# Kernel optimization log

Hardware: AMD Instinct MI355X
Metric: run time of the kernel (lower is better)

The kernel has to match this reference:

```python
import jax, jax.numpy as jnp
import numpy as np

N = 50000      # nodes
E = 1600000    # edges (avg degree 32)
F_IN = 128
HID = 256
C = 40


def setup_inputs() -> dict:
    key = jax.random.key(0)
    ks = jax.random.split(key, 12)
    x = jax.random.normal(ks[0], (N, F_IN), jnp.float32)
    edge_index = jax.random.randint(ks[1], (2, E), 0, N, dtype=jnp.int32)

    def glorot(k, fan_in, fan_out):
        s = jnp.sqrt(2.0 / (fan_in + fan_out)).astype(jnp.float32)
        return jax.random.normal(k, (fan_in, fan_out), jnp.float32) * s

    return {
        "x": x,
        "edge_index": edge_index,
        "W1": glorot(ks[2], F_IN, HID), "b1": jnp.zeros((HID,), jnp.float32),
        "W2": glorot(ks[3], HID, HID),  "b2": jnp.zeros((HID,), jnp.float32),
        "W3": glorot(ks[4], HID, HID),  "b3": jnp.zeros((HID,), jnp.float32),
        "W4": glorot(ks[5], HID, C),    "b4": jnp.zeros((C,), jnp.float32),
    }


def _gcn_conv(x, W, b, src, dst, norm_e, self_norm):
    # PyG GCNConv: h = X W; out_j = sum_i norm_ij * h_i  (+ self-loop term) + b
    h = x @ W                                   # [N, F_out]
    msg = h[src] * norm_e[:, None]              # [E, F_out] gather + scale
    agg = jax.ops.segment_sum(msg, dst, num_segments=N)
    agg = agg + h * self_norm[:, None]          # self-loop contribution
    return agg + b


def reference(x, edge_index, W1, b1, W2, b2, W3, b3, W4, b4):
    src, dst = edge_index[0], edge_index[1]
    # degree on A + I (self-loops added), computed over destination nodes
    deg = jax.ops.segment_sum(jnp.ones((E,), x.dtype), dst, num_segments=N) + 1.0
    inv_sqrt = jax.lax.rsqrt(deg)               # [N]
    norm_e = inv_sqrt[src] * inv_sqrt[dst]      # [E] symmetric norm per edge
    self_norm = inv_sqrt * inv_sqrt             # [N] self-loop norm = 1/deg

    h = jax.nn.relu(_gcn_conv(x, W1, b1, src, dst, norm_e, self_norm))
    h = jax.nn.relu(_gcn_conv(h, W2, b2, src, dst, norm_e, self_norm))
    h = jax.nn.relu(_gcn_conv(h, W3, b3, src, dst, norm_e, self_norm))
    h = _gcn_conv(h, W4, b4, src, dst, norm_e, self_norm)
    return jax.nn.log_softmax(h, axis=1)
```

## Files before the change

kernel.cpp:

```cpp
#include <hip/hip_runtime.h>
#include <hip/hip_fp16.h>
#include <math.h>


typedef _Float16 f16x8 __attribute__((ext_vector_type(8)));
typedef float f32x4 __attribute__((ext_vector_type(4)));

__device__ __forceinline__ __half2 u2h2(unsigned u) {
    union { unsigned u; __half2 h; } v; v.u = u; return v.h;
}
__device__ __forceinline__ unsigned h22u(__half2 h) {
    union { unsigned u; __half2 h; } v; v.h = h; return v.u;
}
__device__ __forceinline__ float hlo(unsigned u) {
    return __half2float(__ushort_as_half((unsigned short)(u & 0xFFFFu)));
}
__device__ __forceinline__ float hhi(unsigned u) {
    return __half2float(__ushort_as_half((unsigned short)(u >> 16)));
}


__global__ __launch_bounds__(256) void count_kernel(const int* __restrict__ dst,
                                                    int* __restrict__ counts,
                                                    int* __restrict__ rank, int E) {
    int e = blockIdx.x * 256 + threadIdx.x;
    if (e < E) rank[e] = atomicAdd(&counts[dst[e]], 1);
}

__global__ __launch_bounds__(256) void scan_phase1(const int* __restrict__ counts,
                                                   int* __restrict__ blockSums, int N) {
    int i = blockIdx.x * 256 + threadIdx.x;
    int v = (i < N) ? counts[i] : 0;
    #pragma unroll
    for (int o = 32; o >= 1; o >>= 1) v += __shfl_xor(v, o, 64);
    __shared__ int ws[4];
    int lane = threadIdx.x & 63, w = threadIdx.x >> 6;
    if (lane == 0) ws[w] = v;
    __syncthreads();
    if (threadIdx.x == 0) blockSums[blockIdx.x] = ws[0] + ws[1] + ws[2] + ws[3];
}

__global__ __launch_bounds__(256) void scan_phase2(int* __restrict__ blockSums, int nb) {
    __shared__ int s[256];
    int tid = threadIdx.x;
    int v = (tid < nb) ? blockSums[tid] : 0;
    s[tid] = v;
    __syncthreads();
    for (int off = 1; off < 256; off <<= 1) {
        int t = (tid >= off) ? s[tid - off] : 0;
        __syncthreads();
        s[tid] += t;
        __syncthreads();
    }
    if (tid < nb) blockSums[tid] = s[tid] - v;
}

__global__ __launch_bounds__(256) void scan_phase3(const int* __restrict__ counts,
                                                   const int* __restrict__ blockSums,
                                                   int* __restrict__ offs,
                                                   float* __restrict__ rsq, int N) {
    __shared__ int s[256];
    int tid = threadIdx.x;
    int i = blockIdx.x * 256 + tid;
    int c = (i < N) ? counts[i] : 0;
    s[tid] = c;
    __syncthreads();
    for (int off = 1; off < 256; off <<= 1) {
        int t = (tid >= off) ? s[tid - off] : 0;
        __syncthreads();
        s[tid] += t;
        __syncthreads();
    }
    if (i < N) {
        int excl = s[tid] - c + blockSums[blockIdx.x];
        offs[i] = excl;
        rsq[i] = rsqrtf((float)c + 1.0f);
        if (i == N - 1) offs[N] = excl + c;
    }
}

__global__ __launch_bounds__(256) void scatter_kernel(const int* __restrict__ src,
                                                      const int* __restrict__ dst,
                                                      const int* __restrict__ rank,
                                                      const int* __restrict__ offs,
                                                      const float* __restrict__ rsq,
                                                      unsigned* __restrict__ epk, int E) {
    int e = blockIdx.x * 256 + threadIdx.x;
    if (e < E) {
        int d = dst[e];
        int s = src[e];
        int pos = offs[d] + rank[e];
        float w = rsq[s] * rsq[d];
        epk[pos] = (unsigned)s |
                   ((unsigned)__half_as_ushort(__float2half_rn(w)) << 16);
    }
}

__global__ __launch_bounds__(256) void prep_kernel(
        const float* __restrict__ x, unsigned short* __restrict__ xb, int nx4,
        const float* __restrict__ W1, const float* __restrict__ W2,
        const float* __restrict__ W3, const float* __restrict__ W4,
        unsigned short* __restrict__ Wt1, unsigned short* __restrict__ Wt2,
        unsigned short* __restrict__ Wt3, unsigned short* __restrict__ Wt4) {
    int i = blockIdx.x * 256 + threadIdx.x;
    if (i < nx4) {
        float4 v = reinterpret_cast<const float4*>(x)[i];
        ushort4 o;
        o.x = __half_as_ushort(__float2half_rn(v.x));
        o.y = __half_as_ushort(__float2half_rn(v.y));
        o.z = __half_as_ushort(__float2half_rn(v.z));
        o.w = __half_as_ushort(__float2half_rn(v.w));
        reinterpret_cast<ushort4*>(xb)[i] = o;
        return;
    }
    int j = i - nx4;
    if (j < 32768) {
        int k = j >> 8, n = j & 255;
        Wt1[n * 128 + k] = __half_as_ushort(__float2half_rn(W1[j]));
    } else if (j < 98304) {
        int t = j - 32768; int k = t >> 8, n = t & 255;
        Wt2[n * 256 + k] = __half_as_ushort(__float2half_rn(W2[t]));
    } else if (j < 163840) {
        int t = j - 98304; int k = t >> 8, n = t & 255;
        Wt3[n * 256 + k] = __half_as_ushort(__float2half_rn(W3[t]));
    } else if (j < 174080) {
        int t = j - 163840; int k = t / 40, n = t - k * 40;
        Wt4[n * 256 + k] = __half_as_ushort(__float2half_rn(W4[t]));
    }
}

template <int H2, bool BIAS, bool RELU>
__global__ __launch_bounds__(256) void agg_f16_kernel(
        const unsigned* __restrict__ G,
        const int* __restrict__ offs,
        const unsigned* __restrict__ epk,
        const float* __restrict__ rsq,
        const float* __restrict__ bias,
        unsigned* __restrict__ out, int N) {
    constexpr int ROWU = 64 * H2;
    constexpr int UNR = 8;
    int lane = threadIdx.x & 63;
    int node = blockIdx.x * 4 + (threadIdx.x >> 6);
    if (node >= N) return;
    const unsigned* base = G + lane * H2;

    __half2 acc[H2];
    #pragma unroll
    for (int i = 0; i < H2; i++) acc[i] = u2h2(0u);

    int e = offs[node], e1 = offs[node + 1];
    for (; e + UNR - 1 < e1; e += UNR) {
        unsigned p[UNR];
        int s[UNR];
        #pragma unroll
        for (int j = 0; j < UNR; j++) { p[j] = epk[e + j]; s[j] = p[j] & 0xFFFFu; }
        unsigned g[UNR][H2];
        #pragma unroll
        for (int j = 0; j < UNR; j++)
            #pragma unroll
            for (int i = 0; i < H2; i++)
                g[j][i] = base[(size_t)s[j] * ROWU + i];
        #pragma unroll
        for (int j = 0; j < UNR; j++) {
            __half2 w2 = __half2half2(__ushort_as_half((unsigned short)(p[j] >> 16)));
            #pragma unroll
            for (int i = 0; i < H2; i++)
                acc[i] = __hfma2(w2, u2h2(g[j][i]), acc[i]);
        }
    }
    for (; e < e1; e++) {
        unsigned p0 = epk[e];
        int s0 = p0 & 0xFFFFu;
        __half2 w2 = __half2half2(__ushort_as_half((unsigned short)(p0 >> 16)));
        #pragma unroll
        for (int i = 0; i < H2; i++)
            acc[i] = __hfma2(w2, u2h2(base[(size_t)s0 * ROWU + i]), acc[i]);
    }

    float sn = rsq[node];
    sn *= sn;
    #pragma unroll
    for (int i = 0; i < H2; i++) {
        unsigned sv = base[(size_t)node * ROWU + i];
        float2 f = __half22float2(acc[i]);
        f.x = fmaf(sn, hlo(sv), f.x);
        f.y = fmaf(sn, hhi(sv), f.y);
        if (BIAS) {
            float2 b = reinterpret_cast<const float2*>(bias)[lane * H2 + i];
            f.x += b.x; f.y += b.y;
        }
        if (RELU) { f.x = fmaxf(f.x, 0.f); f.y = fmaxf(f.y, 0.f); }
        out[(size_t)node * ROWU + lane * H2 + i] = h22u(__floats2half2_rn(f.x, f.y));
    }
}

__global__ __launch_bounds__(256) void agg40_softmax_kernel(
        const unsigned* __restrict__ G,
        const int* __restrict__ offs,
        const unsigned* __restrict__ epk,
        const float* __restrict__ rsq,
        const float* __restrict__ bias,
        float* __restrict__ out, int N) {
    int lane = threadIdx.x & 63;
    int node = blockIdx.x * 4 + (threadIdx.x >> 6);
    if (node >= N) return;
    bool act = lane < 20;
    int cl = act ? lane : 0;
    __half2 acch = u2h2(0u);
    int e = offs[node], e1 = offs[node + 1];
    for (; e + 3 < e1; e += 4) {
        unsigned p[4];
        int s[4];
        #pragma unroll
        for (int j = 0; j < 4; j++) { p[j] = epk[e + j]; s[j] = p[j] & 0xFFFFu; }
        unsigned g[4];
        #pragma unroll
        for (int j = 0; j < 4; j++) g[j] = G[(size_t)s[j] * 20 + cl];
        #pragma unroll
        for (int j = 0; j < 4; j++) {
            __half2 w = __half2half2(__ushort_as_half((unsigned short)(p[j] >> 16)));
            acch = __hfma2(w, u2h2(g[j]), acch);
        }
    }
    for (; e < e1; e++) {
        unsigned p0 = epk[e];
        int s0 = p0 & 0xFFFFu;
        __half2 w0 = __half2half2(__ushort_as_half((unsigned short)(p0 >> 16)));
        acch = __hfma2(w0, u2h2(G[(size_t)s0 * 20 + cl]), acch);
    }
    float lo = 0.f, hi = 0.f;
    if (act) {
        float sn = rsq[node];
        sn *= sn;
        unsigned sv = G[(size_t)node * 20 + lane];
        float2 f = __half22float2(acch);
        lo = fmaf(sn, hlo(sv), f.x) + bias[2 * lane];
        hi = fmaf(sn, hhi(sv), f.y) + bias[2 * lane + 1];
    }
    float m = act ? fmaxf(lo, hi) : -INFINITY;
    #pragma unroll
    for (int o = 32; o >= 1; o >>= 1) m = fmaxf(m, __shfl_xor(m, o, 64));
    float s = act ? (expf(lo - m) + expf(hi - m)) : 0.f;
    #pragma unroll
    for (int o = 32; o >= 1; o >>= 1) s += __shfl_xor(s, o, 64);
    float ls = logf(s);
    if (act) {
        float2 o2;
        o2.x = lo - m - ls;
        o2.y = hi - m - ls;
        *reinterpret_cast<float2*>(out + (size_t)node * 40 + 2 * lane) = o2;
    }
}

template <bool BIAS, bool RELU>
__global__ __launch_bounds__(256) void gemm_f16(
        const unsigned short* __restrict__ A,
        const unsigned short* __restrict__ Bt,
        const float* __restrict__ bias,
        unsigned short* __restrict__ Cout,
        int M, int K, int Nc) {
    __shared__ __align__(16) unsigned short As[128 * 72];
    __shared__ __align__(16) unsigned short Bs[128 * 72];
    int tid = threadIdx.x;
    int lane = tid & 63;
    int wid = tid >> 6;
    int rowBase = blockIdx.y * 128;
    int colBase = blockIdx.x * 128;
    int waveM = (wid & 1) * 64;
    int waveN = (wid >> 1) * 64;

    f32x4 acc[4][4] = {};
    int lrow = lane & 15;
    int kgrp = (lane >> 4) * 8;

    for (int k0 = 0; k0 < K; k0 += 64) {
        #pragma unroll
        for (int i = 0; i < 4; i++) {
            int c = tid + 256 * i;
            int row = c >> 3;
            int kp = (c & 7) * 8;
            int4 av = make_int4(0, 0, 0, 0);
            int gr = rowBase + row;
            if (gr < M)
                av = *reinterpret_cast<const int4*>(A + (size_t)gr * K + k0 + kp);
            *reinterpret_cast<int4*>(&As[row * 72 + kp]) = av;
            int4 bv = make_int4(0, 0, 0, 0);
            int gc = colBase + row;
            if (gc < Nc)
                bv = *reinterpret_cast<const int4*>(Bt + (size_t)gc * K + k0 + kp);
            *reinterpret_cast<int4*>(&Bs[row * 72 + kp]) = bv;
        }
        __syncthreads();
        #pragma unroll
        for (int kk = 0; kk < 64; kk += 32) {
            f16x8 af[4], bfr[4];
            #pragma unroll
            for (int t = 0; t < 4; t++) {
                af[t] = *reinterpret_cast<const f16x8*>(
                    &As[(waveM + t * 16 + lrow) * 72 + kk + kgrp]);
                bfr[t] = *reinterpret_cast<const f16x8*>(
                    &Bs[(waveN + t * 16 + lrow) * 72 + kk + kgrp]);
            }
            #pragma unroll
            for (int mt = 0; mt < 4; mt++)
                #pragma unroll
                for (int nt = 0; nt < 4; nt++)
                    acc[mt][nt] = __builtin_amdgcn_mfma_f32_16x16x32_f16(
                        af[mt], bfr[nt], acc[mt][nt], 0, 0, 0);
        }
        __syncthreads();
    }

    #pragma unroll
    for (int mt = 0; mt < 4; mt++) {
        #pragma unroll
        for (int r = 0; r < 4; r++) {
            int row = rowBase + waveM + mt * 16 + (lane >> 4) * 4 + r;
            if (row >= M) continue;
            #pragma unroll
            for (int nt = 0; nt < 4; nt++) {
                int col = colBase + waveN + nt * 16 + (lane & 15);
                if (col >= Nc) continue;
                float v = acc[mt][nt][r];
                if (BIAS) v += bias[col];
                if (RELU) v = fmaxf(v, 0.f);
                Cout[(size_t)row * Nc + col] = __half_as_ushort(__float2half_rn(v));
            }
        }
    }
}


extern "C" void kernel_launch(void* const* d_in, const int* in_sizes, int n_in,
                              void* d_out, int out_size, void* d_ws, size_t ws_size,
                              hipStream_t stream) {
    const float* x  = (const float*)d_in[0];
    const int*   ei = (const int*)d_in[1];
    const float* W1 = (const float*)d_in[2];
    const float* b1 = (const float*)d_in[3];
    const float* W2 = (const float*)d_in[4];
    const float* b2 = (const float*)d_in[5];
    const float* W3 = (const float*)d_in[6];
    const float* b3 = (const float*)d_in[7];
    const float* W4 = (const float*)d_in[8];
    const float* b4 = (const float*)d_in[9];

    const int FIN = 128, HID = 256, C = 40;
    const int N = in_sizes[0] / FIN;
    const int E = in_sizes[1] / 2;
    const int* src = ei;
    const int* dst = ei + E;

    char* w = (char*)d_ws;
    auto alloc = [&](size_t bytes) {
        char* p = w;
        w += (bytes + 255) & ~(size_t)255;
        return p;
    };
    int nScanBlocks = (N + 255) / 256;
    int*   counts = (int*)alloc((size_t)N * 4);
    int*   offs   = (int*)alloc((size_t)(N + 1) * 4);
    float* rsq    = (float*)alloc((size_t)N * 4);
    int*   bsums  = (int*)alloc((size_t)nScanBlocks * 4);
    int*   rank   = (int*)alloc((size_t)E * 4);
    unsigned* epk = (unsigned*)alloc((size_t)E * 4);
    unsigned short* xb   = (unsigned short*)alloc((size_t)N * FIN * 2);
    unsigned short* aggx = (unsigned short*)alloc((size_t)N * FIN * 2);
    unsigned short* bufA = (unsigned short*)alloc((size_t)N * HID * 2);
    unsigned short* bufB = (unsigned short*)alloc((size_t)N * HID * 2);
    unsigned short* Wt1 = (unsigned short*)alloc((size_t)FIN * HID * 2);
    unsigned short* Wt2 = (unsigned short*)alloc((size_t)HID * HID * 2);
    unsigned short* Wt3 = (unsigned short*)alloc((size_t)HID * HID * 2);
    unsigned short* Wt4 = (unsigned short*)alloc((size_t)HID * C * 2);

    hipMemsetAsync(counts, 0, (size_t)N * 4, stream);

    int nx4 = N * FIN / 4;
    prep_kernel<<<(nx4 + 174080 + 255) / 256, 256, 0, stream>>>(
        x, xb, nx4, W1, W2, W3, W4, Wt1, Wt2, Wt3, Wt4);

    count_kernel<<<(E + 255) / 256, 256, 0, stream>>>(dst, counts, rank, E);
    scan_phase1<<<nScanBlocks, 256, 0, stream>>>(counts, bsums, N);
    scan_phase2<<<1, 256, 0, stream>>>(bsums, nScanBlocks);
    scan_phase3<<<nScanBlocks, 256, 0, stream>>>(counts, bsums, offs, rsq, N);
    scatter_kernel<<<(E + 255) / 256, 256, 0, stream>>>(src, dst, rank, offs, rsq,
                                                        epk, E);

    int grp = (N + 3) / 4;
    dim3 gHID((HID + 127) / 128, (N + 127) / 128);
    dim3 gC((C + 127) / 128, (N + 127) / 128);

    agg_f16_kernel<1, false, false>
        <<<grp, 256, 0, stream>>>((const unsigned*)xb, offs, epk, rsq, nullptr,
                                  (unsigned*)aggx, N);
    gemm_f16<true, true><<<gHID, 256, 0, stream>>>(aggx, Wt1, b1, bufA, N, FIN, HID);
    gemm_f16<false, false><<<gHID, 256, 0, stream>>>(bufA, Wt2, nullptr, bufB,
                                                     N, HID, HID);
    agg_f16_kernel<2, true, true>
        <<<grp, 256, 0, stream>>>((const unsigned*)bufB, offs, epk, rsq, b2,
                                  (unsigned*)bufA, N);
    gemm_f16<false, false><<<gHID, 256, 0, stream>>>(bufA, Wt3, nullptr, bufB,
                                                     N, HID, HID);
    agg_f16_kernel<2, true, true>
        <<<grp, 256, 0, stream>>>((const unsigned*)bufB, offs, epk, rsq, b3,
                                  (unsigned*)bufA, N);
    gemm_f16<false, false><<<gC, 256, 0, stream>>>(bufA, Wt4, nullptr, bufB,
                                                   N, HID, C);
    agg40_softmax_kernel<<<grp, 256, 0, stream>>>((const unsigned*)bufB, offs, epk,
                                                  rsq, b4, (float*)d_out, N);
}
```

Before: 631.9 us.

## Bucket CSR edges by source range and split 256-wide aggregation into column passes

Edges within each destination's CSR segment are now sorted into 8 buckets by source-id range (src>>13). The counts and scan grow to N*8 entries, and a finalize kernel derives per-node offsets and rsqrt degree from them. Each 256-wide aggregation becomes two passes over 128-column halves. Each pass gathers one dword per lane and is meant to keep the gathered source rows more cache-local. This costs a scan eight times larger, an extra kernel, and reading the edge list twice per layer.

```diff
diff --git a/kernel.cpp b/kernel.cpp
--- a/kernel.cpp
+++ b/kernel.cpp
@@ -6,6 +6,9 @@
 typedef _Float16 f16x8 __attribute__((ext_vector_type(8)));
 typedef float f32x4 __attribute__((ext_vector_type(4)));
 
+#define SB 8
+#define SBSHIFT 13
+
 __device__ __forceinline__ __half2 u2h2(unsigned u) {
     union { unsigned u; __half2 h; } v; v.u = u; return v.h;
 }
@@ -20,17 +23,21 @@
 }
 
 
-__global__ __launch_bounds__(256) void count_kernel(const int* __restrict__ dst,
+__global__ __launch_bounds__(256) void count_kernel(const int* __restrict__ src,
+                                                    const int* __restrict__ dst,
                                                     int* __restrict__ counts,
                                                     int* __restrict__ rank, int E) {
     int e = blockIdx.x * 256 + threadIdx.x;
-    if (e < E) rank[e] = atomicAdd(&counts[dst[e]], 1);
+    if (e < E) {
+        int d = dst[e], s = src[e];
+        rank[e] = atomicAdd(&counts[d * SB + (s >> SBSHIFT)], 1);
+    }
 }
 
 __global__ __launch_bounds__(256) void scan_phase1(const int* __restrict__ counts,
-                                                   int* __restrict__ blockSums, int N) {
+                                                   int* __restrict__ blockSums, int NS) {
     int i = blockIdx.x * 256 + threadIdx.x;
-    int v = (i < N) ? counts[i] : 0;
+    int v = (i < NS) ? counts[i] : 0;
     #pragma unroll
     for (int o = 32; o >= 1; o >>= 1) v += __shfl_xor(v, o, 64);
     __shared__ int ws[4];
@@ -40,29 +47,32 @@
     if (threadIdx.x == 0) blockSums[blockIdx.x] = ws[0] + ws[1] + ws[2] + ws[3];
 }
 
-__global__ __launch_bounds__(256) void scan_phase2(int* __restrict__ blockSums, int nb) {
-    __shared__ int s[256];
+__global__ __launch_bounds__(1024) void scan_phase2(int* __restrict__ bs, int nb) {
+    __shared__ int s[1024];
     int tid = threadIdx.x;
-    int v = (tid < nb) ? blockSums[tid] : 0;
-    s[tid] = v;
+    int v0 = (2 * tid < nb) ? bs[2 * tid] : 0;
+    int v1 = (2 * tid + 1 < nb) ? bs[2 * tid + 1] : 0;
+    int ps = v0 + v1;
+    s[tid] = ps;
     __syncthreads();
-    for (int off = 1; off < 256; off <<= 1) {
+    for (int off = 1; off < 1024; off <<= 1) {
         int t = (tid >= off) ? s[tid - off] : 0;
         __syncthreads();
         s[tid] += t;
         __syncthreads();
     }
-    if (tid < nb) blockSums[tid] = s[tid] - v;
+    int excl = s[tid] - ps;
+    if (2 * tid < nb) bs[2 * tid] = excl;
+    if (2 * tid + 1 < nb) bs[2 * tid + 1] = excl + v0;
 }
 
 __global__ __launch_bounds__(256) void scan_phase3(const int* __restrict__ counts,
                                                    const int* __restrict__ blockSums,
-                                                   int* __restrict__ offs,
-                                                   float* __restrict__ rsq, int N) {
+                                                   int* __restrict__ offs2, int NS) {
     __shared__ int s[256];
     int tid = threadIdx.x;
     int i = blockIdx.x * 256 + tid;
-    int c = (i < N) ? counts[i] : 0;
+    int c = (i < NS) ? counts[i] : 0;
     s[tid] = c;
     __syncthreads();
     for (int off = 1; off < 256; off <<= 1) {
@@ -71,25 +81,37 @@
         s[tid] += t;
         __syncthreads();
     }
-    if (i < N) {
+    if (i < NS) {
         int excl = s[tid] - c + blockSums[blockIdx.x];
-        offs[i] = excl;
-        rsq[i] = rsqrtf((float)c + 1.0f);
-        if (i == N - 1) offs[N] = excl + c;
+        offs2[i] = excl;
+        if (i == NS - 1) offs2[NS] = excl + c;
+    }
+}
+
+__global__ __launch_bounds__(256) void finalize_kernel(const int* __restrict__ offs2,
+                                                       int* __restrict__ offs,
+                                                       float* __restrict__ rsq, int N) {
+    int n = blockIdx.x * 256 + threadIdx.x;
+    if (n < N) {
+        int b0 = offs2[n * SB];
+        int b1 = offs2[n * SB + SB];
+        offs[n] = b0;
+        rsq[n] = rsqrtf((float)(b1 - b0) + 1.0f);
+        if (n == N - 1) offs[N] = b1;
     }
 }
 
 __global__ __launch_bounds__(256) void scatter_kernel(const int* __restrict__ src,
                                                       const int* __restrict__ dst,
                                                       const int* __restrict__ rank,
-                                                      const int* __restrict__ offs,
+                                                      const int* __restrict__ offs2,
                                                       const float* __restrict__ rsq,
                                                       unsigned* __restrict__ epk, int E) {
     int e = blockIdx.x * 256 + threadIdx.x;
     if (e < E) {
         int d = dst[e];
         int s = src[e];
-        int pos = offs[d] + rank[e];
+        int pos = offs2[d * SB + (s >> SBSHIFT)] + rank[e];
         float w = rsq[s] * rsq[d];
         epk[pos] = (unsigned)s |
                    ((unsigned)__half_as_ushort(__float2half_rn(w)) << 16);
@@ -129,69 +151,55 @@
     }
 }
 
-template <int H2, bool BIAS, bool RELU>
-__global__ __launch_bounds__(256) void agg_f16_kernel(
+template <int ROWU, bool BIAS, bool RELU>
+__global__ __launch_bounds__(256) void agg_pass_kernel(
         const unsigned* __restrict__ G,
         const int* __restrict__ offs,
         const unsigned* __restrict__ epk,
         const float* __restrict__ rsq,
         const float* __restrict__ bias,
-        unsigned* __restrict__ out, int N) {
-    constexpr int ROWU = 64 * H2;
+        unsigned* __restrict__ out, int N, int colOff) {
     constexpr int UNR = 8;
     int lane = threadIdx.x & 63;
     int node = blockIdx.x * 4 + (threadIdx.x >> 6);
     if (node >= N) return;
-    const unsigned* base = G + lane * H2;
-
-    __half2 acc[H2];
-    #pragma unroll
-    for (int i = 0; i < H2; i++) acc[i] = u2h2(0u);
-
+    const unsigned* base = G + colOff + lane;
+
+    __half2 acc = u2h2(0u);
     int e = offs[node], e1 = offs[node + 1];
     for (; e + UNR - 1 < e1; e += UNR) {
         unsigned p[UNR];
         int s[UNR];
         #pragma unroll
         for (int j = 0; j < UNR; j++) { p[j] = epk[e + j]; s[j] = p[j] & 0xFFFFu; }
-        unsigned g[UNR][H2];
-        #pragma unroll
-        for (int j = 0; j < UNR; j++)
-            #pragma unroll
-            for (int i = 0; i < H2; i++)
-                g[j][i] = base[(size_t)s[j] * ROWU + i];
+        unsigned g[UNR];
+        #pragma unroll
+        for (int j = 0; j < UNR; j++) g[j] = base[(size_t)s[j] * ROWU];
         #pragma unroll
         for (int j = 0; j < UNR; j++) {
             __half2 w2 = __half2half2(__ushort_as_half((unsigned short)(p[j] >> 16)));
-            #pragma unroll
-            for (int i = 0; i < H2; i++)
-                acc[i] = __hfma2(w2, u2h2(g[j][i]), acc[i]);
+            acc = __hfma2(w2, u2h2(g[j]), acc);
         }
     }
     for (; e < e1; e++) {
         unsigned p0 = epk[e];
         int s0 = p0 & 0xFFFFu;
         __half2 w2 = __half2half2(__ushort_as_half((unsigned short)(p0 >> 16)));
-        #pragma unroll
-        for (int i = 0; i < H2; i++)
-            acc[i] = __hfma2(w2, u2h2(base[(size_t)s0 * ROWU + i]), acc[i]);
+        acc = __hfma2(w2, u2h2(base[(size_t)s0 * ROWU]), acc);
     }
 
     float sn = rsq[node];
     sn *= sn;
-    #pragma unroll
-    for (int i = 0; i < H2; i++) {
-        unsigned sv = base[(size_t)node * ROWU + i];
-        float2 f = __half22float2(acc[i]);
-        f.x = fmaf(sn, hlo(sv), f.x);
-        f.y = fmaf(sn, hhi(sv), f.y);
-        if (BIAS) {
-            float2 b = reinterpret_cast<const float2*>(bias)[lane * H2 + i];
-            f.x += b.x; f.y += b.y;
-        }
-        if (RELU) { f.x = fmaxf(f.x, 0.f); f.y = fmaxf(f.y, 0.f); }
-        out[(size_t)node * ROWU + lane * H2 + i] = h22u(__floats2half2_rn(f.x, f.y));
-    }
+    unsigned sv = base[(size_t)node * ROWU];
+    float2 f = __half22float2(acc);
+    f.x = fmaf(sn, hlo(sv), f.x);
+    f.y = fmaf(sn, hhi(sv), f.y);
+    if (BIAS) {
+        float2 b = reinterpret_cast<const float2*>(bias)[colOff + lane];
+        f.x += b.x; f.y += b.y;
+    }
+    if (RELU) { f.x = fmaxf(f.x, 0.f); f.y = fmaxf(f.y, 0.f); }
+    out[(size_t)node * ROWU + colOff + lane] = h22u(__floats2half2_rn(f.x, f.y));
 }
 
 __global__ __launch_bounds__(256) void agg40_softmax_kernel(
@@ -350,6 +358,7 @@
     const int E = in_sizes[1] / 2;
     const int* src = ei;
     const int* dst = ei + E;
+    const int NS = N * SB;
 
     char* w = (char*)d_ws;
     auto alloc = [&](size_t bytes) {
@@ -357,8 +366,9 @@
         w += (bytes + 255) & ~(size_t)255;
         return p;
     };
-    int nScanBlocks = (N + 255) / 256;
-    int*   counts = (int*)alloc((size_t)N * 4);
+    int nScanBlocks = (NS + 255) / 256;
+    int*   counts = (int*)alloc((size_t)NS * 4);
+    int*   offs2  = (int*)alloc((size_t)(NS + 1) * 4);
     int*   offs   = (int*)alloc((size_t)(N + 1) * 4);
     float* rsq    = (float*)alloc((size_t)N * 4);
     int*   bsums  = (int*)alloc((size_t)nScanBlocks * 4);
@@ -373,37 +383,44 @@
     unsigned short* Wt3 = (unsigned short*)alloc((size_t)HID * HID * 2);
     unsigned short* Wt4 = (unsigned short*)alloc((size_t)HID * C * 2);
 
-    hipMemsetAsync(counts, 0, (size_t)N * 4, stream);
+    hipMemsetAsync(counts, 0, (size_t)NS * 4, stream);
 
     int nx4 = N * FIN / 4;
     prep_kernel<<<(nx4 + 174080 + 255) / 256, 256, 0, stream>>>(
         x, xb, nx4, W1, W2, W3, W4, Wt1, Wt2, Wt3, Wt4);
 
-    count_kernel<<<(E + 255) / 256, 256, 0, stream>>>(dst, counts, rank, E);
-    scan_phase1<<<nScanBlocks, 256, 0, stream>>>(counts, bsums, N);
-    scan_phase2<<<1, 256, 0, stream>>>(bsums, nScanBlocks);
-    scan_phase3<<<nScanBlocks, 256, 0, stream>>>(counts, bsums, offs, rsq, N);
-    scatter_kernel<<<(E + 255) / 256, 256, 0, stream>>>(src, dst, rank, offs, rsq,
+    count_kernel<<<(E + 255) / 256, 256, 0, stream>>>(src, dst, counts, rank, E);
+    scan_phase1<<<nScanBlocks, 256, 0, stream>>>(counts, bsums, NS);
+    scan_phase2<<<1, 1024, 0, stream>>>(bsums, nScanBlocks);
+    scan_phase3<<<nScanBlocks, 256, 0, stream>>>(counts, bsums, offs2, NS);
+    finalize_kernel<<<(N + 255) / 256, 256, 0, stream>>>(offs2, offs, rsq, N);
+    scatter_kernel<<<(E + 255) / 256, 256, 0, stream>>>(src, dst, rank, offs2, rsq,
                                                         epk, E);
 
     int grp = (N + 3) / 4;
     dim3 gHID((HID + 127) / 128, (N + 127) / 128);
     dim3 gC((C + 127) / 128, (N + 127) / 128);
 
-    agg_f16_kernel<1, false, false>
+    agg_pass_kernel<64, false, false>
         <<<grp, 256, 0, stream>>>((const unsigned*)xb, offs, epk, rsq, nullptr,
-                                  (unsigned*)aggx, N);
+                                  (unsigned*)aggx, N, 0);
     gemm_f16<true, true><<<gHID, 256, 0, stream>>>(aggx, Wt1, b1, bufA, N, FIN, HID);
     gemm_f16<false, false><<<gHID, 256, 0, stream>>>(bufA, Wt2, nullptr, bufB,
                                                      N, HID, HID);
-    agg_f16_kernel<2, true, true>
+    agg_pass_kernel<128, true, true>
         <<<grp, 256, 0, stream>>>((const unsigned*)bufB, offs, epk, rsq, b2,
-                                  (unsigned*)bufA, N);
+                                  (unsigned*)bufA, N, 0);
+    agg_pass_kernel<128, true, true>
+        <<<grp, 256, 0, stream>>>((const unsigned*)bufB, offs, epk, rsq, b2,
+                                  (unsigned*)bufA, N, 64);
     gemm_f16<false, false><<<gHID, 256, 0, stream>>>(bufA, Wt3, nullptr, bufB,
                                                      N, HID, HID);
-    agg_f16_kernel<2, true, true>
+    agg_pass_kernel<128, true, true>
         <<<grp, 256, 0, stream>>>((const unsigned*)bufB, offs, epk, rsq, b3,
-                                  (unsigned*)bufA, N);
+                                  (unsigned*)bufA, N, 0);
+    agg_pass_kernel<128, true, true>
+        <<<grp, 256, 0, stream>>>((const unsigned*)bufB, offs, epk, rsq, b3,
+                                  (unsigned*)bufA, N, 64);
     gemm_f16<false, false><<<gC, 256, 0, stream>>>(bufA, Wt4, nullptr, bufB,
                                                    N, HID, C);
     agg40_softmax_kernel<<<grp, 256, 0, stream>>>((const unsigned*)bufB, offs, epk,
```

New measurement: 638.5 us. Within noise of the previous version (+1.1%).
